# Performance work log

Hardware: AMD Instinct MI355X
Metric: run time of the kernel (lower is better)

## Reference

```python
import jax, jax.numpy as jnp
import numpy as np

VOCAB_SIZE = 50257


def setup_inputs() -> dict:
    key = jax.random.key(0)
    B, S = 512, 2048
    assignments = jax.random.randint(key, (B, S), 0, VOCAB_SIZE, dtype=jnp.int64)
    # ones_w are the unit weights scattered into the histogram; counting ones == counting occurrences.
    ones_w = jnp.ones((B, S), dtype=jnp.float32)
    return {"assignments": assignments, "ones_w": ones_w}


def reference(assignments, ones_w):
    # Per-row vocab histogram via scatter-add (avoids the O(B*S*V) broadcast-compare
    # intermediate of the original torch code; same math).
    B, S = assignments.shape
    rows = jnp.arange(B)[:, None]                          # (B, 1) broadcast against (B, S)
    counts = jnp.zeros((B, VOCAB_SIZE), dtype=ones_w.dtype).at[rows, assignments].add(ones_w)
    # Normalize each row's histogram to a frequency distribution.
    frequency = counts / jnp.sum(counts, axis=-1, keepdims=True)
    return frequency
```

## Files before the change

kernel.cpp:

```cpp
#include <hip/hip_runtime.h>

#define VOCAB 50257
#define NCH   8
#define CHUNK 6284
#define BLK   256

typedef float f32x4 __attribute__((ext_vector_type(4)));

#define LDS_BARRIER()                                            \
    do {                                                         \
        asm volatile("s_waitcnt lgkmcnt(0)" ::: "memory");       \
        __builtin_amdgcn_s_barrier();                            \
        __builtin_amdgcn_sched_barrier(0);                       \
    } while (0)

__global__ __launch_bounds__(BLK) void XTermFrequency_5471788335935_kernel(
    const int* __restrict__ asg, const float* __restrict__ w,
    float* __restrict__ out, int S, int B)
{
    __shared__ f32x4 hist4[CHUNK / 4];
    __shared__ float s_sum;
    float* hist = reinterpret_cast<float*>(hist4);

    const int bid = blockIdx.x;
    const int c   = bid / B;
    const int r   = bid - c * B;
    const int lo  = c * CHUNK;
    const int hi  = min(CHUNK, VOCAB - lo);

    const int tid = threadIdx.x;
    const int*   __restrict__ row  = asg + (long long)r * S;
    const float* __restrict__ wrow = w   + (long long)r * S;
    float*       __restrict__ po   = out + (long long)r * VOCAB + lo;

    const f32x4 z4 = {0.f, 0.f, 0.f, 0.f};
    for (int j = tid; j < CHUNK / 4; j += BLK) hist4[j] = z4;
    if (tid == 0) s_sum = 0.f;
    __syncthreads();

    float ws = 0.f;
    if ((S & 3) == 0) {
        const int4*   __restrict__ rv = reinterpret_cast<const int4*>(row);
        const float4* __restrict__ wv = reinterpret_cast<const float4*>(wrow);
        for (int q = tid; q < (S >> 2); q += BLK) {
            const int4   a4 = rv[q];
            const float4 w4 = wv[q];
            ws += (w4.x + w4.y) + (w4.z + w4.w);
            const int v0 = a4.x - lo, v1 = a4.y - lo,
                      v2 = a4.z - lo, v3 = a4.w - lo;
            if ((unsigned)v0 < (unsigned)CHUNK) atomicAdd(&hist[v0], w4.x);
            if ((unsigned)v1 < (unsigned)CHUNK) atomicAdd(&hist[v1], w4.y);
            if ((unsigned)v2 < (unsigned)CHUNK) atomicAdd(&hist[v2], w4.z);
            if ((unsigned)v3 < (unsigned)CHUNK) atomicAdd(&hist[v3], w4.w);
        }
    } else {
        for (int s = tid; s < S; s += BLK) {
            ws += wrow[s];
            const int v = row[s] - lo;
            if ((unsigned)v < (unsigned)CHUNK) atomicAdd(&hist[v], wrow[s]);
        }
    }
    #pragma unroll
    for (int off = 32; off > 0; off >>= 1) ws += __shfl_down(ws, off, 64);
    if ((tid & 63) == 0) atomicAdd(&s_sum, ws);
    LDS_BARRIER();

    const float inv = 1.0f / s_sum;

    const int head0 = (int)(((16u - ((unsigned)(uintptr_t)po & 15u)) & 15u) >> 2);
    const int head  = head0 < hi ? head0 : hi;
    if (tid < head) po[tid] = hist[tid] * inv;
    const int nv = (hi - head) >> 2;
    float4* __restrict__ pv = reinterpret_cast<float4*>(po + head);
    for (int j = tid; j < nv; j += BLK) {
        const int i = head + (j << 2);
        float4 h;
        h.x = hist[i]     * inv;
        h.y = hist[i + 1] * inv;
        h.z = hist[i + 2] * inv;
        h.w = hist[i + 3] * inv;
        pv[j] = h;
    }
    for (int i = head + (nv << 2) + tid; i < hi; i += BLK)
        po[i] = hist[i] * inv;
}

extern "C" void kernel_launch(void* const* d_in, const int* in_sizes, int n_in,
                              void* d_out, int out_size, void* d_ws, size_t ws_size,
                              hipStream_t stream) {
    const int*   asg = (const int*)d_in[0];
    const float* w   = (const float*)d_in[1];
    float*       out = (float*)d_out;

    const int B = out_size / VOCAB;
    const int S = in_sizes[0] / B;

    XTermFrequency_5471788335935_kernel<<<B * NCH, BLK, 0, stream>>>(
        asg, w, out, S, B);
}
```

Before: 24.68 us.

## Use single-wave blocks without barriers and nontemporal vector stores

```diff
diff --git a/kernel.cpp b/kernel.cpp
--- a/kernel.cpp
+++ b/kernel.cpp
@@ -3,46 +3,38 @@
 #define VOCAB 50257
 #define NCH   8
 #define CHUNK 6284
-#define BLK   256
+#define NV4   (CHUNK / 4)
 
 typedef float f32x4 __attribute__((ext_vector_type(4)));
 
-#define LDS_BARRIER()                                            \
-    do {                                                         \
-        asm volatile("s_waitcnt lgkmcnt(0)" ::: "memory");       \
-        __builtin_amdgcn_s_barrier();                            \
-        __builtin_amdgcn_sched_barrier(0);                       \
-    } while (0)
-
-__global__ __launch_bounds__(BLK) void XTermFrequency_5471788335935_kernel(
+__global__ __launch_bounds__(64) void XTermFrequency_5471788335935_kernel(
     const int* __restrict__ asg, const float* __restrict__ w,
     float* __restrict__ out, int S, int B)
 {
-    __shared__ f32x4 hist4[CHUNK / 4];
-    __shared__ float s_sum;
+    __shared__ f32x4 hist4[NV4];
     float* hist = reinterpret_cast<float*>(hist4);
 
-    const int bid = blockIdx.x;
-    const int c   = bid / B;
-    const int r   = bid - c * B;
-    const int lo  = c * CHUNK;
-    const int hi  = min(CHUNK, VOCAB - lo);
+    const int bid  = blockIdx.x;
+    const int c    = bid / B;
+    const int r    = bid - c * B;
+    const int lo   = c * CHUNK;
+    const int hi   = min(CHUNK, VOCAB - lo);
+    const int lane = threadIdx.x;
 
-    const int tid = threadIdx.x;
     const int*   __restrict__ row  = asg + (long long)r * S;
     const float* __restrict__ wrow = w   + (long long)r * S;
     float*       __restrict__ po   = out + (long long)r * VOCAB + lo;
 
     const f32x4 z4 = {0.f, 0.f, 0.f, 0.f};
-    for (int j = tid; j < CHUNK / 4; j += BLK) hist4[j] = z4;
-    if (tid == 0) s_sum = 0.f;
-    __syncthreads();
+    for (int j = lane; j < NV4; j += 64) hist4[j] = z4;
+    asm volatile("s_waitcnt lgkmcnt(0)" ::: "memory");
 
     float ws = 0.f;
     if ((S & 3) == 0) {
         const int4*   __restrict__ rv = reinterpret_cast<const int4*>(row);
         const float4* __restrict__ wv = reinterpret_cast<const float4*>(wrow);
-        for (int q = tid; q < (S >> 2); q += BLK) {
+        const int nq = S >> 2;
+        for (int q = lane; q < nq; q += 64) {
             const int4   a4 = rv[q];
             const float4 w4 = wv[q];
             ws += (w4.x + w4.y) + (w4.z + w4.w);
@@ -54,35 +46,33 @@
             if ((unsigned)v3 < (unsigned)CHUNK) atomicAdd(&hist[v3], w4.w);
         }
     } else {
-        for (int s = tid; s < S; s += BLK) {
-            ws += wrow[s];
+        for (int s = lane; s < S; s += 64) {
+            const float ww = wrow[s];
+            ws += ww;
             const int v = row[s] - lo;
-            if ((unsigned)v < (unsigned)CHUNK) atomicAdd(&hist[v], wrow[s]);
+            if ((unsigned)v < (unsigned)CHUNK) atomicAdd(&hist[v], ww);
         }
     }
+
     #pragma unroll
-    for (int off = 32; off > 0; off >>= 1) ws += __shfl_down(ws, off, 64);
-    if ((tid & 63) == 0) atomicAdd(&s_sum, ws);
-    LDS_BARRIER();
+    for (int off = 1; off < 64; off <<= 1) ws += __shfl_xor(ws, off, 64);
+    const float inv = 1.0f / ws;
 
-    const float inv = 1.0f / s_sum;
+    asm volatile("s_waitcnt lgkmcnt(0)" ::: "memory");
 
-    const int head0 = (int)(((16u - ((unsigned)(uintptr_t)po & 15u)) & 15u) >> 2);
-    const int head  = head0 < hi ? head0 : hi;
-    if (tid < head) po[tid] = hist[tid] * inv;
-    const int nv = (hi - head) >> 2;
-    float4* __restrict__ pv = reinterpret_cast<float4*>(po + head);
-    for (int j = tid; j < nv; j += BLK) {
-        const int i = head + (j << 2);
-        float4 h;
-        h.x = hist[i]     * inv;
-        h.y = hist[i + 1] * inv;
-        h.z = hist[i + 2] * inv;
-        h.w = hist[i + 3] * inv;
-        pv[j] = h;
+    const int nv = hi >> 2;
+    for (int j = lane; j < nv; j += 64) {
+        f32x4 h = hist4[j] * inv;
+        float* p = po + (j << 2);
+        asm volatile("global_store_dwordx4 %0, %1, off nt"
+                     :: "v"(p), "v"(h));
     }
-    for (int i = head + (nv << 2) + tid; i < hi; i += BLK)
-        po[i] = hist[i] * inv;
+    for (int i = (nv << 2) + lane; i < hi; i += 64) {
+        float h = hist[i] * inv;
+        float* p = po + i;
+        asm volatile("global_store_dword %0, %1, off nt"
+                     :: "v"(p), "v"(h));
+    }
 }
 
 extern "C" void kernel_launch(void* const* d_in, const int* in_sizes, int n_in,
@@ -95,6 +85,6 @@
     const int B = out_size / VOCAB;
     const int S = in_sizes[0] / B;
 
-    XTermFrequency_5471788335935_kernel<<<B * NCH, BLK, 0, stream>>>(
+    XTermFrequency_5471788335935_kernel<<<B * NCH, 64, 0, stream>>>(
         asg, w, out, S, B);
 }
```

Result: slower. 32.19 us (+30.4%).
